# Performance work log

Measured on AMD Instinct MI355X. Metric: run time of the kernel, lower is better.

## Reference

```python
import jax, jax.numpy as jnp
from jax import lax
import numpy as np

P = 0.25  # dropouto


def _lstm(x, Wih, Whh, b):
    """Standard torch-layout LSTM over [B, T, I]; gate order i,f,g,o.
    Wih: [4H, I], Whh: [4H, H], b: [4H] (= b_ih + b_hh). Returns [B, T, H]."""
    B, T, I = x.shape
    H = Whh.shape[1]
    # Precompute input contributions for all timesteps in one GEMM.
    xg = jnp.einsum('bti,gi->btg', x, Wih) + b  # [B, T, 4H]
    xg = jnp.swapaxes(xg, 0, 1)  # [T, B, 4H]

    def step(carry, xt):
        h, c = carry
        g = xt + h @ Whh.T  # [B, 4H]
        i, f, gg, o = jnp.split(g, 4, axis=-1)
        i = jax.nn.sigmoid(i)
        f = jax.nn.sigmoid(f)
        gg = jnp.tanh(gg)
        o = jax.nn.sigmoid(o)
        c = f * c + i * gg
        h = o * jnp.tanh(c)
        return (h, c), h

    h0 = jnp.zeros((B, H), x.dtype)
    c0 = jnp.zeros((B, H), x.dtype)
    _, hs = lax.scan(step, (h0, c0), xg)  # hs: [T, B, H]
    return jnp.swapaxes(hs, 0, 1)


def setup_inputs() -> dict:
    key = jax.random.key(0)
    ks = jax.random.split(key, 10)
    B, T = 512, 4096
    H1, H2 = 16, 1
    s = 0.25  # small init scale
    x = jax.random.normal(ks[0], (B, T, 1), jnp.float32)
    Wih1 = jax.random.normal(ks[1], (4 * H1, 1), jnp.float32) * s
    Whh1 = jax.random.normal(ks[2], (4 * H1, H1), jnp.float32) * s
    b1 = jax.random.normal(ks[3], (4 * H1,), jnp.float32) * s
    Wih2 = jax.random.normal(ks[4], (4 * H2, H1), jnp.float32) * s
    Whh2 = jax.random.normal(ks[5], (4 * H2, H2), jnp.float32) * s
    b2 = jax.random.normal(ks[6], (4 * H2,), jnp.float32) * s
    keep = 1.0 - P
    # Variational dropout masks: one mask per sequence, shared over time.
    mask1 = jax.random.bernoulli(ks[7], keep, (B, 1, H1)).astype(jnp.float32) / keep
    mask2 = jax.random.bernoulli(ks[8], keep, (B, 1, H2)).astype(jnp.float32) / keep
    return {"x": x, "Wih1": Wih1, "Whh1": Whh1, "b1": b1,
            "Wih2": Wih2, "Whh2": Whh2, "b2": b2,
            "mask1": mask1, "mask2": mask2}


def reference(x, Wih1, Whh1, b1, Wih2, Whh2, b2, mask1, mask2):
    out = _lstm(x, Wih1, Whh1, b1) * mask1   # dropouto on lstm1 output
    out = _lstm(out, Wih2, Whh2, b2) * mask2  # dropouto on lstm2 output
    return out  # [B, T, 1]
```

## Files before the change

kernel.cpp:

```cpp
#include <hip/hip_runtime.h>


static __device__ __forceinline__ float rdlane(float v, int l) {
  return __uint_as_float(__builtin_amdgcn_readlane(__float_as_uint(v), (unsigned)l));
}

template <int CTRL>
static __device__ __forceinline__ float qperm(float v) {
  return __uint_as_float(__builtin_amdgcn_update_dpp(
      0u, __float_as_uint(v), CTRL, 0xF, 0xF, true));
}

static __device__ __forceinline__ float exp2a(float x) {
  float r;
  asm("v_exp_f32 %0, %1" : "=v"(r) : "v"(x));
  return r;
}
static __device__ __forceinline__ float rcpa(float x) {
  return __builtin_amdgcn_rcpf(x);
}

#define QP_BC0 0x00
#define QP_BC1 0x55
#define QP_BC2 0xAA
#define QP_BC3 0xFF

__global__ __launch_bounds__(64, 1) void vdd_lstm_kernel(
    const float* __restrict__ x,
    const float* __restrict__ Wih1,
    const float* __restrict__ Whh1,
    const float* __restrict__ b1,
    const float* __restrict__ Wih2,
    const float* __restrict__ Whh2,
    const float* __restrict__ b2,
    const float* __restrict__ mask1,
    const float* __restrict__ mask2,
    float* __restrict__ out,
    int T) {
  const int b = blockIdx.x;
  const int lane = threadIdx.x;
  const int j = lane >> 2;
  const int gt = lane & 3;
  const int row = gt * 16 + j;

  const float LOG2E = 1.4426950408889634f;
  const bool isg = (gt == 2);
  const float sc = isg ? (-2.f * LOG2E) : (-LOG2E);
  const float aA = isg ? (-4.f * LOG2E) : 1.f;
  const float aC = isg ? (2.f * LOG2E) : 0.f;

  float w[16];
#pragma unroll
  for (int k = 0; k < 16; ++k) w[k] = Whh1[row * 16 + k] * sc;
  const float wih1 = Wih1[row] * sc;
  const float bb1  = b1[row] * sc;
  float w2m[16];
#pragma unroll
  for (int k = 0; k < 16; ++k) w2m[k] = Wih2[gt * 16 + k] * mask1[b * 16 + k] * sc;
  const float whh2 = Whh2[gt] * sc;
  const float bb2  = b2[gt] * sc;
  const float m2   = mask2[b];

  const float* xb = x + (size_t)b * T;
  float* ob = out + (size_t)b * T;

  float h = 0.f, cs = 0.f;
  float cs2 = 0.f, h2b = 0.f;

  float xcur = xb[lane];
  const int NCH = T >> 6;

  {
    float sx = rdlane(xcur, 0);
    float pre = __fmaf_rn(wih1, sx, bb1);
    float a1 = __fmaf_rn(aA, rcpa(1.f + exp2a(pre)), aC);
    float i1 = qperm<QP_BC0>(a1);
    float g1 = qperm<QP_BC2>(a1);
    float o1 = qperm<QP_BC3>(a1);
    cs = i1 * g1;
    h = o1 * __fmaf_rn(2.f, rcpa(1.f + exp2a(cs)), -1.f);
  }

  for (int ch = 0; ch < NCH; ++ch) {
    int nb = (ch + 1) << 6;
    nb = (nb + 64 <= T) ? nb : 0;
    float xnext = xb[nb + lane];

    float och = 0.f;

#pragma unroll 8
    for (int s = 0; s < 64; ++s) {
      float xsrc = (s < 63) ? xcur : xnext;
      float sx = rdlane(xsrc, (s + 1) & 63);

      float sh[16];
#pragma unroll
      for (int k = 0; k < 16; ++k) sh[k] = rdlane(h, 4 * k);

      float p0 = __fmaf_rn(wih1, sx, bb1);
      p0 = __fmaf_rn(w[0], sh[0], p0);
      float p1 = w[1] * sh[1];
      float p2 = w[2] * sh[2];
      float p3 = w[3] * sh[3];
#pragma unroll
      for (int k = 4; k < 16; k += 4) {
        p0 = __fmaf_rn(w[k + 0], sh[k + 0], p0);
        p1 = __fmaf_rn(w[k + 1], sh[k + 1], p1);
        p2 = __fmaf_rn(w[k + 2], sh[k + 2], p2);
        p3 = __fmaf_rn(w[k + 3], sh[k + 3], p3);
      }
      float pre = (p0 + p1) + (p2 + p3);

      float q0 = __fmaf_rn(whh2, h2b, bb2);
      q0 = __fmaf_rn(w2m[0], sh[0], q0);
      float q1 = w2m[1] * sh[1];
      float q2 = w2m[2] * sh[2];
      float q3 = w2m[3] * sh[3];
#pragma unroll
      for (int k = 4; k < 16; k += 4) {
        q0 = __fmaf_rn(w2m[k + 0], sh[k + 0], q0);
        q1 = __fmaf_rn(w2m[k + 1], sh[k + 1], q1);
        q2 = __fmaf_rn(w2m[k + 2], sh[k + 2], q2);
        q3 = __fmaf_rn(w2m[k + 3], sh[k + 3], q3);
      }
      float pre2 = (q0 + q1) + (q2 + q3);

      float a1 = __fmaf_rn(aA, rcpa(1.f + exp2a(pre)), aC);
      float i1 = qperm<QP_BC0>(a1);
      float f1 = qperm<QP_BC1>(a1);
      float g1 = qperm<QP_BC2>(a1);
      float o1 = qperm<QP_BC3>(a1);
      cs = __fmaf_rn(f1, cs, i1 * g1);
      float hn = o1 * __fmaf_rn(2.f, rcpa(1.f + exp2a(cs)), -1.f);

      float a2 = __fmaf_rn(aA, rcpa(1.f + exp2a(pre2)), aC);
      float i2 = qperm<QP_BC0>(a2);
      float f2 = qperm<QP_BC1>(a2);
      float g2 = qperm<QP_BC2>(a2);
      float o2 = qperm<QP_BC3>(a2);
      cs2 = __fmaf_rn(f2, cs2, i2 * g2);
      h2b = o2 * __fmaf_rn(2.f, rcpa(1.f + exp2a(cs2)), -1.f);
      float ov = h2b * m2;

      och = (lane == s) ? ov : och;
      h = hn;
    }

    ob[(ch << 6) + lane] = och;
    xcur = xnext;
  }
}

extern "C" void kernel_launch(void* const* d_in, const int* in_sizes, int n_in,
                              void* d_out, int out_size, void* d_ws, size_t ws_size,
                              hipStream_t stream) {
  const float* x     = (const float*)d_in[0];
  const float* Wih1  = (const float*)d_in[1];
  const float* Whh1  = (const float*)d_in[2];
  const float* b1    = (const float*)d_in[3];
  const float* Wih2  = (const float*)d_in[4];
  const float* Whh2  = (const float*)d_in[5];
  const float* b2    = (const float*)d_in[6];
  const float* mask1 = (const float*)d_in[7];
  const float* mask2 = (const float*)d_in[8];
  float* out = (float*)d_out;

  const int B = in_sizes[8];
  const int T = in_sizes[0] / B;

  vdd_lstm_kernel<<<dim3(B), dim3(64), 0, stream>>>(
      x, Wih1, Whh1, b1, Wih2, Whh2, b2, mask1, mask2, out, T);
}
```

Before: 670.9 us.

## Pack hidden state to fp16 pairs and use dot2 for recurrent matvecs

Each step packs adjacent h values into fp16 pairs with a ds_swizzle plus cvt_pkrtz. This halves the per-step readlane broadcasts from 16 to 8, and the two 16-wide matvecs now use v_dot2_f32_f16 instead of scalar FMAs. The x prefetch is reindexed so one readlane per step fetches x[t+1], removing the per-step select. The cost is reduced precision, since weights and hidden state are rounded to fp16, and the swizzle adds LDS-path latency to the serial recurrence.

Result: faster. 641.1 us (-4.5%).

```diff
diff --git a/kernel.cpp b/kernel.cpp
--- a/kernel.cpp
+++ b/kernel.cpp
@@ -1,8 +1,12 @@
 #include <hip/hip_runtime.h>
 
+typedef __fp16 f16x2 __attribute__((ext_vector_type(2)));
 
 static __device__ __forceinline__ float rdlane(float v, int l) {
   return __uint_as_float(__builtin_amdgcn_readlane(__float_as_uint(v), (unsigned)l));
+}
+static __device__ __forceinline__ unsigned rdlane_u(unsigned v, int l) {
+  return __builtin_amdgcn_readlane(v, (unsigned)l);
 }
 
 template <int CTRL>
@@ -18,6 +22,17 @@
 }
 static __device__ __forceinline__ float rcpa(float x) {
   return __builtin_amdgcn_rcpf(x);
+}
+
+static __device__ __forceinline__ float dot2f(f16x2 a, unsigned bu, float c) {
+#if __has_builtin(__builtin_amdgcn_fdot2)
+  return __builtin_amdgcn_fdot2(a, __builtin_bit_cast(f16x2, bu), c, false);
+#else
+  float r = c;
+  f16x2 b = __builtin_bit_cast(f16x2, bu);
+  asm("v_dot2_f32_f16 %0, %1, %2, %0" : "+v"(r) : "v"(a), "v"(b));
+  return r;
+#endif
 }
 
 #define QP_BC0 0x00
@@ -49,14 +64,20 @@
   const float aA = isg ? (-4.f * LOG2E) : 1.f;
   const float aC = isg ? (2.f * LOG2E) : 0.f;
 
-  float w[16];
+  f16x2 wh1[8];
 #pragma unroll
-  for (int k = 0; k < 16; ++k) w[k] = Whh1[row * 16 + k] * sc;
+  for (int m = 0; m < 8; ++m) {
+    wh1[m].x = (__fp16)(Whh1[row * 16 + 2 * m] * sc);
+    wh1[m].y = (__fp16)(Whh1[row * 16 + 2 * m + 1] * sc);
+  }
+  f16x2 wh2[8];
+#pragma unroll
+  for (int m = 0; m < 8; ++m) {
+    wh2[m].x = (__fp16)(Wih2[gt * 16 + 2 * m] * mask1[b * 16 + 2 * m] * sc);
+    wh2[m].y = (__fp16)(Wih2[gt * 16 + 2 * m + 1] * mask1[b * 16 + 2 * m + 1] * sc);
+  }
   const float wih1 = Wih1[row] * sc;
   const float bb1  = b1[row] * sc;
-  float w2m[16];
-#pragma unroll
-  for (int k = 0; k < 16; ++k) w2m[k] = Wih2[gt * 16 + k] * mask1[b * 16 + k] * sc;
   const float whh2 = Whh2[gt] * sc;
   const float bb2  = b2[gt] * sc;
   const float m2   = mask2[b];
@@ -67,12 +88,15 @@
   float h = 0.f, cs = 0.f;
   float cs2 = 0.f, h2b = 0.f;
 
-  float xcur = xb[lane];
   const int NCH = T >> 6;
+  const int tmax = T - 1;
+
+  int idx0 = 1 + lane; idx0 = idx0 > tmax ? tmax : idx0;
+  float xr = xb[idx0];
 
   {
-    float sx = rdlane(xcur, 0);
-    float pre = __fmaf_rn(wih1, sx, bb1);
+    float x0 = xb[0];
+    float pre = __fmaf_rn(wih1, x0, bb1);
     float a1 = __fmaf_rn(aA, rcpa(1.f + exp2a(pre)), aC);
     float i1 = qperm<QP_BC0>(a1);
     float g1 = qperm<QP_BC2>(a1);
@@ -82,48 +106,46 @@
   }
 
   for (int ch = 0; ch < NCH; ++ch) {
-    int nb = (ch + 1) << 6;
-    nb = (nb + 64 <= T) ? nb : 0;
-    float xnext = xb[nb + lane];
+    int idxn = (ch + 1) * 64 + 1 + lane;
+    idxn = idxn > tmax ? tmax : idxn;
+    float xnext = xb[idxn];
 
     float och = 0.f;
 
 #pragma unroll 8
     for (int s = 0; s < 64; ++s) {
-      float xsrc = (s < 63) ? xcur : xnext;
-      float sx = rdlane(xsrc, (s + 1) & 63);
+      unsigned hsw = (unsigned)__builtin_amdgcn_ds_swizzle(
+          (int)__float_as_uint(h), 0x101F);
+      f16x2 tp = __builtin_bit_cast(
+          f16x2, __builtin_amdgcn_cvt_pkrtz(h, __uint_as_float(hsw)));
+      unsigned tpu = __builtin_bit_cast(unsigned, tp);
+      unsigned sp[8];
+#pragma unroll
+      for (int m = 0; m < 8; ++m) sp[m] = rdlane_u(tpu, 8 * m);
 
-      float sh[16];
-#pragma unroll
-      for (int k = 0; k < 16; ++k) sh[k] = rdlane(h, 4 * k);
+      float sx = rdlane(xr, s);
 
-      float p0 = __fmaf_rn(wih1, sx, bb1);
-      p0 = __fmaf_rn(w[0], sh[0], p0);
-      float p1 = w[1] * sh[1];
-      float p2 = w[2] * sh[2];
-      float p3 = w[3] * sh[3];
-#pragma unroll
-      for (int k = 4; k < 16; k += 4) {
-        p0 = __fmaf_rn(w[k + 0], sh[k + 0], p0);
-        p1 = __fmaf_rn(w[k + 1], sh[k + 1], p1);
-        p2 = __fmaf_rn(w[k + 2], sh[k + 2], p2);
-        p3 = __fmaf_rn(w[k + 3], sh[k + 3], p3);
-      }
-      float pre = (p0 + p1) + (p2 + p3);
+      float accA = __fmaf_rn(wih1, sx, bb1);
+      float accB = dot2f(wh1[1], sp[1], 0.f);
+      accA = dot2f(wh1[0], sp[0], accA);
+      accB = dot2f(wh1[3], sp[3], accB);
+      accA = dot2f(wh1[2], sp[2], accA);
+      accB = dot2f(wh1[5], sp[5], accB);
+      accA = dot2f(wh1[4], sp[4], accA);
+      accB = dot2f(wh1[7], sp[7], accB);
+      accA = dot2f(wh1[6], sp[6], accA);
+      float pre = accA + accB;
 
-      float q0 = __fmaf_rn(whh2, h2b, bb2);
-      q0 = __fmaf_rn(w2m[0], sh[0], q0);
-      float q1 = w2m[1] * sh[1];
-      float q2 = w2m[2] * sh[2];
-      float q3 = w2m[3] * sh[3];
-#pragma unroll
-      for (int k = 4; k < 16; k += 4) {
-        q0 = __fmaf_rn(w2m[k + 0], sh[k + 0], q0);
-        q1 = __fmaf_rn(w2m[k + 1], sh[k + 1], q1);
-        q2 = __fmaf_rn(w2m[k + 2], sh[k + 2], q2);
-        q3 = __fmaf_rn(w2m[k + 3], sh[k + 3], q3);
-      }
-      float pre2 = (q0 + q1) + (q2 + q3);
+      float accC = __fmaf_rn(whh2, h2b, bb2);
+      float accD = dot2f(wh2[1], sp[1], 0.f);
+      accC = dot2f(wh2[0], sp[0], accC);
+      accD = dot2f(wh2[3], sp[3], accD);
+      accC = dot2f(wh2[2], sp[2], accC);
+      accD = dot2f(wh2[5], sp[5], accD);
+      accC = dot2f(wh2[4], sp[4], accC);
+      accD = dot2f(wh2[7], sp[7], accD);
+      accC = dot2f(wh2[6], sp[6], accC);
+      float pre2 = accC + accD;
 
       float a1 = __fmaf_rn(aA, rcpa(1.f + exp2a(pre)), aC);
       float i1 = qperm<QP_BC0>(a1);
@@ -147,7 +169,7 @@
     }
 
     ob[(ch << 6) + lane] = och;
-    xcur = xnext;
+    xr = xnext;
   }
 }
 
```
